# Optimization experiments

Measured on AMD Instinct MI355X. Metric: run time of the kernel, lower is better.

Reference implementation:

```python
import jax, jax.numpy as jnp
import numpy as np

LR = 0.01            # learning_rate
PC = 0.001           # pred_clipping
WC = 5.0             # weight_clipping
_LO = float(np.log(PC / (1.0 - PC)))   # logit(pred_clipping)
_HI = -_LO                              # logit(1 - pred_clipping)


def setup_inputs() -> dict:
    B, S, I, CTX, M, C = 64, 1023, 1024, 784, 4, 1  # S = size-1 (bias row), C = num_classes->1
    key = jax.random.key(0)
    k = jax.random.split(key, 6)
    logit = jax.random.normal(k[0], (B, I, C), jnp.float32)
    context = jax.random.normal(k[1], (B, CTX), jnp.float32)
    target = jax.random.uniform(k[2], (B, C), dtype=jnp.float32)
    cm = jax.random.normal(k[3], (C, S, M, CTX), jnp.float32)
    cm = cm / jnp.linalg.norm(cm, axis=-1, keepdims=True)          # unit-norm context maps
    cb = jax.random.normal(k[4], (C, S, M, 1), jnp.float32)        # context bias
    weights = jnp.full((C, S, 2 ** M, I), 1.0 / I, jnp.float32)    # per-context weight table
    bias = jax.random.uniform(k[5], (1, 1, C), jnp.float32, _LO, _HI)
    return {"logit": logit, "context": context, "target": target,
            "context_maps": cm, "context_bias": cb, "weights": weights, "bias": bias}


def reference(logit, context, target, context_maps, context_bias, weights, bias):
    C, S, M, _ = context_maps.shape
    B = context.shape[0]
    # halfspace hashing of the context -> per-(class, neuron, sample) weight-table index
    dist = jnp.einsum('csmk,bk->csmb', context_maps, context)      # [C,S,M,B]
    bits = (dist > context_bias).astype(jnp.int32)
    conv = (2 ** jnp.arange(M, dtype=jnp.int32))[:, None]          # [M,1]
    idx = jnp.sum(bits * conv, axis=-2)                            # [C,S,B] in [0, 2^M)
    ci = jnp.arange(C)[:, None, None]
    si = jnp.arange(S)[None, :, None]
    sel = weights[ci, si, idx]                                     # gather -> [C,S,B,I]
    # batched dot product (torch code does full matmul + diagonal; this is the same math)
    out = jnp.clip(jnp.einsum('csbi,bic->csb', sel, logit), _LO, _HI)
    out_bsc = out.transpose(2, 1, 0)                               # [B,S,C]
    # online weight update (target branch): gather-compute-scatter
    diff = jax.nn.sigmoid(out_bsc) - target[:, None, :]            # [B,S,C]
    upd = LR * diff[..., None] * logit.transpose(0, 2, 1)[:, None, :, :]  # [B,S,C,I]
    new_sel = jnp.clip(sel - upd.transpose(2, 1, 0, 3), -WC, WC)   # [C,S,B,I]
    new_weights = weights.at[ci, si, idx].set(new_sel)             # scatter
    # prepend constant bias neuron
    out_logits = jnp.concatenate([jnp.broadcast_to(bias, (B, 1, C)), out_bsc], axis=1)  # [B,S+1,C]
    return out_logits, new_weights
```

## Files before the change

kernel.cpp:

```cpp
#include <hip/hip_runtime.h>
#include <math.h>

typedef unsigned long long u64;
typedef __attribute__((ext_vector_type(8))) short bf16x8;
typedef __attribute__((ext_vector_type(4))) float f32x4;

#define S_DIM 1023
#define B_DIM 64
#define I_DIM 1024
#define CTX_DIM 784
#define CTX4 196
#define NWROWS 16

#define LR_C 0.01f
#define WC_C 5.0f
#define LO_C (-6.906754778648554f)
#define HI_C ( 6.906754778648554f)

__device__ __forceinline__ float dot4(float4 a, float4 b) {
    return a.x * b.x + a.y * b.y + a.z * b.z + a.w * b.w;
}

__device__ __forceinline__ float4 upd4(float4 w, float4 a, float c) {
    float4 r;
    r.x = fminf(fmaxf(w.x - c * a.x, -WC_C), WC_C);
    r.y = fminf(fmaxf(w.y - c * a.y, -WC_C), WC_C);
    r.z = fminf(fmaxf(w.z - c * a.z, -WC_C), WC_C);
    r.w = fminf(fmaxf(w.w - c * a.w, -WC_C), WC_C);
    return r;
}

__device__ __forceinline__ short f2bf(float f) {
    union { float f; unsigned u; } cv; cv.f = f;
    unsigned r = cv.u + 0x7fffu + ((cv.u >> 16) & 1u);
    return (short)(r >> 16);
}

__global__ __launch_bounds__(256) void prep_pack_kernel(
    const float* __restrict__ context,
    const float* __restrict__ bias,
    const float* __restrict__ logit,
    float4* __restrict__ ctxT4,
    short* __restrict__ pack_b,
    float* __restrict__ out_logits)
{
    const int blk = blockIdx.x;
    const int t = threadIdx.x;
    if (blk < 49) {
        int g = blk * 256 + t;
        int k4 = g >> 6;
        int b  = g & 63;
        ctxT4[g] = *(const float4*)(context + (size_t)b * CTX_DIM + k4 * 4);
        if (g < B_DIM) out_logits[(size_t)g * (S_DIM + 1)] = bias[0];
    } else {
        int g = (blk - 49) * 256 + t;
        int l  = g & 63;
        int kb = (g >> 6) & 31;
        int nt = g >> 11;
        int b  = nt * 16 + (l & 15);
        int i0 = kb * 32 + (l >> 4) * 8;
        const float* src = logit + (size_t)b * I_DIM + i0;
        bf16x8 v;
        #pragma unroll
        for (int j = 0; j < 8; ++j) v[j] = f2bf(src[j]);
        *(bf16x8*)(pack_b + (size_t)g * 8) = v;
    }
}

__global__ __launch_bounds__(256, 4) void gln_one_kernel(
    const float* __restrict__ logit,
    const float* __restrict__ target,
    const float* __restrict__ weights,
    const float* __restrict__ cm,
    const float* __restrict__ cb,
    const float4* __restrict__ ctxT4,
    const short* __restrict__ pack_b,
    float* __restrict__ out_logits,
    float* __restrict__ new_weights)
{
    __shared__ short Abf[NWROWS * I_DIM];
    __shared__ float red[4][4][64];
    __shared__ int   bits[4][64];
    __shared__ float cb_lds[4];
    __shared__ u64   mask_lds[NWROWS];
    __shared__ int   lastb_lds[NWROWS];
    __shared__ float coef_lds[NWROWS];

    const int s  = blockIdx.x;
    const int t  = threadIdx.x;
    const int wv = t >> 6;
    const int l  = t & 63;

    const float4* W4 = (const float4*)(weights + (size_t)s * (NWROWS * I_DIM));
    float4 Wr[16];
    #pragma unroll
    for (int j = 0; j < 16; ++j) Wr[j] = W4[t + j * 256];
    __builtin_amdgcn_sched_barrier(0);

    if (t < 4) cb_lds[t] = cb[s * 4 + t];

    {
        const int b = t & 63;
        const int q = __builtin_amdgcn_readfirstlane(t >> 6);
        const float4* cmr = (const float4*)(cm + (size_t)s * 4 * CTX_DIM);
        float a0 = 0.f, a1 = 0.f, a2 = 0.f, a3 = 0.f;
        const int k0 = q * 49;
        #pragma unroll 7
        for (int kk = 0; kk < 49; ++kk) {
            int k4 = k0 + kk;
            float4 c4 = ctxT4[k4 * 64 + b];
            a0 += dot4(cmr[k4], c4);
            a1 += dot4(cmr[CTX4 + k4], c4);
            a2 += dot4(cmr[2 * CTX4 + k4], c4);
            a3 += dot4(cmr[3 * CTX4 + k4], c4);
        }
        red[q][0][b] = a0;
        red[q][1][b] = a1;
        red[q][2][b] = a2;
        red[q][3][b] = a3;
    }
    __syncthreads();
    {
        int m = t >> 6, bb = t & 63;
        float sum = red[0][m][bb] + red[1][m][bb] + red[2][m][bb] + red[3][m][bb];
        bits[m][bb] = (sum > cb_lds[m]) ? 1 : 0;
    }
    __syncthreads();
    if (t < B_DIM) {
        int v = bits[0][t] + 2 * bits[1][t] + 4 * bits[2][t] + 8 * bits[3][t];
        u64 my = 0;
        #pragma unroll
        for (int kk = 0; kk < NWROWS; ++kk) {
            u64 mk = __ballot(v == kk);
            if (t == kk) my = mk;
        }
        if (t < NWROWS) {
            mask_lds[t]  = my;
            lastb_lds[t] = my ? (63 - __clzll(my)) : -1;
        }
    }

    #pragma unroll
    for (int j = 0; j < 16; ++j) {
        int slot = j * 128 + ((t >> 1) ^ (j & 7));
        short4 v;
        v.x = f2bf(Wr[j].x); v.y = f2bf(Wr[j].y);
        v.z = f2bf(Wr[j].z); v.w = f2bf(Wr[j].w);
        *(short4*)(Abf + slot * 8 + (t & 1) * 4) = v;
    }
    __syncthreads();

    const int row = l & 15;
    const int q2  = l >> 4;
    const int sw  = row & 7;
    const int base_slot = row * 128;
    const bf16x8* Bb = (const bf16x8*)pack_b + (size_t)wv * 2048 + l;
    f32x4 acc = {0.f, 0.f, 0.f, 0.f};
    #pragma unroll 8
    for (int kb = 0; kb < 32; ++kb) {
        bf16x8 af = *(const bf16x8*)(Abf + 8 * (base_slot + ((kb * 4 + q2) ^ sw)));
        bf16x8 bfr = Bb[(size_t)kb * 64];
        acc = __builtin_amdgcn_mfma_f32_16x16x32_bf16(af, bfr, acc, 0, 0, 0);
    }

    const int col = wv * 16 + (l & 15);
    #pragma unroll
    for (int j = 0; j < 4; ++j) {
        int r = q2 * 4 + j;
        u64 m = mask_lds[r];
        if ((m >> col) & 1) {
            float o = fminf(fmaxf(acc[j], LO_C), HI_C);
            out_logits[(size_t)col * (S_DIM + 1) + s + 1] = o;
            if (col == lastb_lds[r])
                coef_lds[r] = LR_C * (1.0f / (1.0f + expf(-o)) - target[col]);
        }
    }
    __syncthreads();

    float4*       D4 = (float4*)(new_weights + (size_t)s * (NWROWS * I_DIM));
    const float4* L4 = (const float4*)logit;
    #pragma unroll
    for (int r = 0; r < NWROWS; ++r) {
        const int lb = lastb_lds[r];
        float4 o;
        if (lb < 0) {
            o = Wr[r];
        } else {
            o = upd4(Wr[r], L4[lb * 256 + t], coef_lds[r]);
        }
        D4[r * 256 + t] = o;
    }
}

extern "C" void kernel_launch(void* const* d_in, const int* in_sizes, int n_in,
                              void* d_out, int out_size, void* d_ws, size_t ws_size,
                              hipStream_t stream) {
    const float* logit   = (const float*)d_in[0];
    const float* context = (const float*)d_in[1];
    const float* target  = (const float*)d_in[2];
    const float* cm      = (const float*)d_in[3];
    const float* cb      = (const float*)d_in[4];
    const float* weights = (const float*)d_in[5];
    const float* bias    = (const float*)d_in[6];

    float* out_logits  = (float*)d_out;
    float* new_weights = out_logits + (size_t)B_DIM * (S_DIM + 1);

    char* ws = (char*)d_ws;
    float4* ctxT4 = (float4*)ws;     ws += (size_t)CTX4 * B_DIM * 16;
    short*  packb = (short*)ws;

    prep_pack_kernel<<<81, 256, 0, stream>>>(context, bias, logit, ctxT4, packb, out_logits);
    gln_one_kernel<<<S_DIM, 256, 0, stream>>>(logit, target, weights, cm, cb,
                                              ctxT4, packb, out_logits, new_weights);
}
```

Measured before the change: 56.57 us.

## Split fused kernel into dot-product kernel and separate weight-update kernel

The single per-neuron kernel, which held the 16 weight rows in registers for the whole run, becomes two kernels. The first converts weights to bf16 in LDS, computes the hashes and dot products, and writes last-sample indices and update coefficients to workspace. A second grid-stride kernel then rereads the weights from global memory and writes the clipped updated table. This frees registers in the first kernel and may improve occupancy, at the cost of reading the 64 MB weight table a second time plus an extra launch.

```diff
diff --git a/kernel.cpp b/kernel.cpp
--- a/kernel.cpp
+++ b/kernel.cpp
@@ -11,6 +11,7 @@
 #define CTX_DIM 784
 #define CTX4 196
 #define NWROWS 16
+#define NTASK (S_DIM * NWROWS)
 
 #define LR_C 0.01f
 #define WC_C 5.0f
@@ -67,7 +68,7 @@
     }
 }
 
-__global__ __launch_bounds__(256, 4) void gln_one_kernel(
+__global__ __launch_bounds__(256, 4) void gln_dots_kernel(
     const float* __restrict__ logit,
     const float* __restrict__ target,
     const float* __restrict__ weights,
@@ -76,7 +77,8 @@
     const float4* __restrict__ ctxT4,
     const short* __restrict__ pack_b,
     float* __restrict__ out_logits,
-    float* __restrict__ new_weights)
+    int*   __restrict__ lastb_g,
+    float* __restrict__ coef_g)
 {
     __shared__ short Abf[NWROWS * I_DIM];
     __shared__ float red[4][4][64];
@@ -84,20 +86,23 @@
     __shared__ float cb_lds[4];
     __shared__ u64   mask_lds[NWROWS];
     __shared__ int   lastb_lds[NWROWS];
-    __shared__ float coef_lds[NWROWS];
 
     const int s  = blockIdx.x;
     const int t  = threadIdx.x;
     const int wv = t >> 6;
     const int l  = t & 63;
 
+    if (t < 4) cb_lds[t] = cb[s * 4 + t];
+
     const float4* W4 = (const float4*)(weights + (size_t)s * (NWROWS * I_DIM));
-    float4 Wr[16];
     #pragma unroll
-    for (int j = 0; j < 16; ++j) Wr[j] = W4[t + j * 256];
-    __builtin_amdgcn_sched_barrier(0);
-
-    if (t < 4) cb_lds[t] = cb[s * 4 + t];
+    for (int j = 0; j < NWROWS; ++j) {
+        float4 w = W4[t + j * 256];
+        int slot = j * 128 + ((t >> 1) ^ (j & 7));
+        short4 v;
+        v.x = f2bf(w.x); v.y = f2bf(w.y); v.z = f2bf(w.z); v.w = f2bf(w.w);
+        *(short4*)(Abf + slot * 8 + (t & 1) * 4) = v;
+    }
 
     {
         const int b = t & 63;
@@ -135,18 +140,11 @@
             if (t == kk) my = mk;
         }
         if (t < NWROWS) {
+            int lb = my ? (63 - __clzll(my)) : -1;
             mask_lds[t]  = my;
-            lastb_lds[t] = my ? (63 - __clzll(my)) : -1;
-        }
-    }
-
-    #pragma unroll
-    for (int j = 0; j < 16; ++j) {
-        int slot = j * 128 + ((t >> 1) ^ (j & 7));
-        short4 v;
-        v.x = f2bf(Wr[j].x); v.y = f2bf(Wr[j].y);
-        v.z = f2bf(Wr[j].z); v.w = f2bf(Wr[j].w);
-        *(short4*)(Abf + slot * 8 + (t & 1) * 4) = v;
+            lastb_lds[t] = lb;
+            lastb_g[s * NWROWS + t] = lb;
+        }
     }
     __syncthreads();
 
@@ -172,23 +170,34 @@
             float o = fminf(fmaxf(acc[j], LO_C), HI_C);
             out_logits[(size_t)col * (S_DIM + 1) + s + 1] = o;
             if (col == lastb_lds[r])
-                coef_lds[r] = LR_C * (1.0f / (1.0f + expf(-o)) - target[col]);
-        }
-    }
-    __syncthreads();
-
-    float4*       D4 = (float4*)(new_weights + (size_t)s * (NWROWS * I_DIM));
-    const float4* L4 = (const float4*)logit;
-    #pragma unroll
-    for (int r = 0; r < NWROWS; ++r) {
-        const int lb = lastb_lds[r];
-        float4 o;
+                coef_g[s * NWROWS + r] = LR_C * (1.0f / (1.0f + expf(-o)) - target[col]);
+        }
+    }
+}
+
+__global__ __launch_bounds__(256) void gln_upd_kernel(
+    const float* __restrict__ logit,
+    const float* __restrict__ weights,
+    const int*   __restrict__ lastb_g,
+    const float* __restrict__ coef_g,
+    float* __restrict__ new_weights)
+{
+    const int total = NTASK * 256;
+    const int stride = gridDim.x * 256;
+    for (int g = blockIdx.x * 256 + threadIdx.x; g < total; g += stride) {
+        const int task = g >> 8;
+        const int off  = g & 255;
+        const int lb   = lastb_g[task];
+        float4 w = ((const float4*)weights)[g];
+        float4 r;
         if (lb < 0) {
-            o = Wr[r];
+            r = w;
         } else {
-            o = upd4(Wr[r], L4[lb * 256 + t], coef_lds[r]);
-        }
-        D4[r * 256 + t] = o;
+            const float c = coef_g[task];
+            float4 a = ((const float4*)logit)[lb * 256 + off];
+            r = upd4(w, a, c);
+        }
+        ((float4*)new_weights)[g] = r;
     }
 }
 
@@ -207,10 +216,14 @@
     float* new_weights = out_logits + (size_t)B_DIM * (S_DIM + 1);
 
     char* ws = (char*)d_ws;
-    float4* ctxT4 = (float4*)ws;     ws += (size_t)CTX4 * B_DIM * 16;
-    short*  packb = (short*)ws;
+    float4* ctxT4   = (float4*)ws;   ws += (size_t)CTX4 * B_DIM * 16;
+    short*  packb   = (short*)ws;    ws += (size_t)4 * 32 * 64 * 8 * 2;
+    int*    lastb_g = (int*)ws;      ws += (size_t)NTASK * 4;
+    float*  coef_g  = (float*)ws;
 
     prep_pack_kernel<<<81, 256, 0, stream>>>(context, bias, logit, ctxT4, packb, out_logits);
-    gln_one_kernel<<<S_DIM, 256, 0, stream>>>(logit, target, weights, cm, cb,
-                                              ctxT4, packb, out_logits, new_weights);
-}
+    gln_dots_kernel<<<S_DIM, 256, 0, stream>>>(logit, target, weights, cm, cb,
+                                               ctxT4, packb, out_logits,
+                                               lastb_g, coef_g);
+    gln_upd_kernel<<<8192, 256, 0, stream>>>(logit, weights, lastb_g, coef_g, new_weights);
+}
```

Result: slower. 64.28 us (+13.6%).
